# Kernel tuning notes

Hardware: AMD Instinct MI355X
Metric: run time of the kernel (lower is better)

## Reference

```python
import jax, jax.numpy as jnp
import numpy as np

EMBED = 1024
NUM_HEADS = 16
HEAD = EMBED // NUM_HEADS  # 64


def setup_inputs() -> dict:
    key = jax.random.key(0)
    kx, kk, kq, kv = jax.random.split(key, 4)
    B, T = 4, 4096
    scale = 1.0 / np.sqrt(EMBED)
    x = jax.random.normal(kx, (B, T, EMBED), dtype=jnp.float32)
    # nn.Linear(embed, head, bias=False) stores weight [head, embed]
    Wk = jax.random.normal(kk, (HEAD, EMBED), dtype=jnp.float32) * scale
    Wq = jax.random.normal(kq, (HEAD, EMBED), dtype=jnp.float32) * scale
    Wv = jax.random.normal(kv, (HEAD, EMBED), dtype=jnp.float32) * scale
    return {"x": x, "Wk": Wk, "Wq": Wq, "Wv": Wv}


def reference(x, Wk, Wq, Wv):
    # x: [B, T, C]; W*: [H, C] (torch Linear layout, y = x @ W.T)
    k = jnp.einsum('btc,hc->bth', x, Wk)  # [B, T, H]
    q = jnp.einsum('btc,hc->bth', x, Wq)
    v = jnp.einsum('btc,hc->bth', x, Wv)
    scale = k.shape[-1] ** -0.5
    wei = jnp.einsum('bth,bsh->bts', q, k) * scale  # [B, T, T]
    wei = jax.nn.softmax(wei, axis=-1)  # no causal mask in source
    out = jnp.einsum('bts,bsh->bth', wei, v)  # [B, T, H]
    return out
```

## Files before the change

kernel.cpp:

```cpp
#include <hip/hip_runtime.h>
#include <hip/hip_bf16.h>
#include <cstdint>

#define TSEQ 4096
#define NB   4
#define HD   64
#define CEMB 1024
#define NQ   8
#define KVCH (TSEQ / NQ)
#define NTOK (NB * TSEQ)
#define SCL  0.18033688011112042f
#define FM   16.0f

typedef __attribute__((ext_vector_type(8)))  short bfrag;
typedef __attribute__((ext_vector_type(4)))  float f4;
typedef __attribute__((ext_vector_type(16))) float f16v;

#define MFMA16(a, b, c) __builtin_amdgcn_mfma_f32_16x16x32_bf16(a, b, c, 0, 0, 0)
#define MFMA32(a, b, c) __builtin_amdgcn_mfma_f32_32x32x16_bf16(a, b, c, 0, 0, 0)

static __device__ __forceinline__ unsigned short f2bf(float f) {
    __hip_bfloat16 h = __float2bfloat16(f);
    return __builtin_bit_cast(unsigned short, h);
}

static __device__ __forceinline__ float bf2f(unsigned short u) {
    const unsigned v = (unsigned)u << 16;
    return __builtin_bit_cast(float, v);
}

static __device__ __forceinline__ unsigned cvtpk(float lo, float hi) {
    unsigned r;
    asm("v_cvt_pk_bf16_f32 %0, %1, %2" : "=v"(r) : "v"(lo), "v"(hi));
    return r;
}

static __device__ __forceinline__ bfrag cvt8pk(const float4 a, const float4 b) {
    uint4 o;
    o.x = cvtpk(a.x, a.y);
    o.y = cvtpk(a.z, a.w);
    o.z = cvtpk(b.x, b.y);
    o.w = cvtpk(b.z, b.w);
    return __builtin_bit_cast(bfrag, o);
}


__global__ __launch_bounds__(256) void wcvt_kernel(
    const float* __restrict__ Wq, const float* __restrict__ Wk,
    const float* __restrict__ Wv, unsigned short* __restrict__ wb)
{
    const int row = blockIdx.x;
    const int col = threadIdx.x * 4;
    const float* W = (row < 64) ? Wq + (size_t)row * CEMB
                   : (row < 128) ? Wk + (size_t)(row - 64) * CEMB
                   : Wv + (size_t)(row - 128) * CEMB;
    const float4 v = *reinterpret_cast<const float4*>(W + col);
    ushort4 o;
    o.x = f2bf(v.x); o.y = f2bf(v.y); o.z = f2bf(v.z); o.w = f2bf(v.w);
    *reinterpret_cast<ushort4*>(wb + (size_t)row * CEMB + col) = o;
}

__global__ __launch_bounds__(256) void proj_kernel(
    const float* __restrict__ x, const unsigned short* __restrict__ wb,
    unsigned short* __restrict__ qb, unsigned short* __restrict__ kf,
    unsigned short* __restrict__ vf)
{
    __shared__ __attribute__((aligned(16))) unsigned short xs[2][32 * 64];
    __shared__ __attribute__((aligned(16))) unsigned short ws[2][192 * 64];

    const int tid  = threadIdx.x;
    const int w    = tid >> 6;
    const int lane = tid & 63;
    const int ln15 = lane & 15, lg = lane >> 4;
    const int rowg = (w >> 1) * 16;
    const int colg = (w & 1) * 96;
    const int rowbase = blockIdx.x * 32;

    f4 acc[6];
    #pragma unroll
    for (int j = 0; j < 6; ++j) acc[j] = f4{0.f, 0.f, 0.f, 0.f};

    const int xrow = tid >> 3;
    const int xs8  = tid & 7;
    const int xswz = (xrow & 7) << 4;

    float4 xf0, xf1;
    bfrag  wf[6];
    auto LOADP = [&](int k0) {
        const float* xsrc = x + (size_t)(rowbase + xrow) * CEMB + k0 + xs8 * 8;
        xf0 = reinterpret_cast<const float4*>(xsrc)[0];
        xf1 = reinterpret_cast<const float4*>(xsrc)[1];
        #pragma unroll
        for (int i = 0; i < 6; ++i) {
            const int seg = tid + i * 256;
            const int srow = seg >> 3, sc = seg & 7;
            wf[i] = *reinterpret_cast<const bfrag*>(wb + (size_t)srow * CEMB + k0 + sc * 8);
        }
    };
    auto WRITEP = [&](int c) {
        char* xd = (char*)xs[c];
        char* wd = (char*)ws[c];
        const bfrag xb = cvt8pk(xf0, xf1);
        *reinterpret_cast<bfrag*>(xd + xrow * 128 + ((xs8 * 16) ^ xswz)) = xb;
        #pragma unroll
        for (int i = 0; i < 6; ++i) {
            const int seg = tid + i * 256;
            const int srow = seg >> 3, sc = seg & 7;
            *reinterpret_cast<bfrag*>(wd + srow * 128 + ((sc * 16) ^ ((srow & 7) << 4))) = wf[i];
        }
    };

    LOADP(0);
    WRITEP(0);
    __syncthreads();

    for (int ch = 0; ch < 16; ++ch) {
        const int c = ch & 1;
        if (ch < 15) LOADP((ch + 1) * 64);

        const char* xp = (const char*)xs[c];
        const char* wp = (const char*)ws[c];
        __builtin_amdgcn_s_setprio(1);
        #pragma unroll
        for (int ks = 0; ks < 2; ++ks) {
            const int cb = ks * 64 + lg * 16;
            const int r0 = rowg + ln15;
            const bfrag a0 = *reinterpret_cast<const bfrag*>(xp + r0 * 128 + (cb ^ ((r0 & 7) << 4)));
            #pragma unroll
            for (int ct = 0; ct < 6; ++ct) {
                const int wr = colg + ct * 16 + ln15;
                const bfrag b = *reinterpret_cast<const bfrag*>(wp + wr * 128 + (cb ^ ((wr & 7) << 4)));
                acc[ct] = MFMA16(a0, b, acc[ct]);
            }
        }
        __builtin_amdgcn_s_setprio(0);

        if (ch < 15) WRITEP(c ^ 1);
        __syncthreads();
    }

    #pragma unroll
    for (int ct = 0; ct < 6; ++ct) {
        const int c = colg + ct * 16 + ln15;
        #pragma unroll
        for (int r = 0; r < 4; ++r) {
            const int grow = rowbase + rowg + 4 * lg + r;
            const int bbi = grow >> 12, t = grow & 4095;
            const int tile = t >> 6, kvr = t & 63;
            if (c < 64) {
                qb[(size_t)grow * HD + c] = f2bf(acc[ct][r] * SCL);
            } else if (c < 128) {
                const int d = c - 64;
                const unsigned short bv16 = f2bf(acc[ct][r]);
                const int lane2 = (kvr & 31) + 32 * ((d >> 3) & 1);
                const size_t idx =
                    ((((size_t)bbi * 64 + tile) * 4 + (d >> 4)) * 2 + (kvr >> 5)) * 512
                    + lane2 * 8 + (d & 7);
                kf[idx] = bv16;
            } else {
                const int d = c - 128;
                const unsigned short bv16 = f2bf(acc[ct][r]);
                const int lane2 = (d & 31) + 32 * ((kvr >> 3) & 1);
                const size_t idx =
                    ((((size_t)bbi * 64 + tile) * 4 + (kvr >> 4)) * 2 + (d >> 5)) * 512
                    + lane2 * 8 + (kvr & 7);
                vf[idx] = bv16;
            }
        }
    }
}

__global__ __launch_bounds__(256, 3) void attn_kernel(
    const unsigned short* __restrict__ qb, const unsigned short* __restrict__ kf,
    const unsigned short* __restrict__ vf, uint2* __restrict__ po2,
    float* __restrict__ pl)
{
    __shared__ __attribute__((aligned(16))) unsigned short kl[2][4096];
    __shared__ __attribute__((aligned(16))) unsigned short vl[2][4096];

    const int tid  = threadIdx.x;
    const int w    = tid >> 6;
    const int lane = tid & 63;
    const int ql   = lane & 31;
    const int hi   = lane >> 5;
    const int chunk = blockIdx.x;
    const int xg    = blockIdx.y;
    const int q0   = xg * 128 + w * 32;
    const int bb   = xg >> 5;
    const int tbase = bb * 64 + chunk * 8;

    bfrag aq[4];
    #pragma unroll
    for (int s = 0; s < 4; ++s)
        aq[s] = *reinterpret_cast<const bfrag*>(
            qb + (size_t)(q0 + ql) * HD + 16 * s + 8 * hi);

    const unsigned short* kg = kf + (size_t)tbase * 4096 + tid * 8;
    const unsigned short* vg = vf + (size_t)tbase * 4096 + tid * 8;

    bfrag sk0, sk1, sv0, sv1;
    auto LOADT = [&](int it) {
        const size_t o = (size_t)it * 4096;
        sk0 = *reinterpret_cast<const bfrag*>(kg + o);
        sk1 = *reinterpret_cast<const bfrag*>(kg + o + 2048);
        sv0 = *reinterpret_cast<const bfrag*>(vg + o);
        sv1 = *reinterpret_cast<const bfrag*>(vg + o + 2048);
    };
    auto WRITET = [&](int c) {
        *reinterpret_cast<bfrag*>(&kl[c][tid * 8]) = sk0;
        *reinterpret_cast<bfrag*>(&kl[c][2048 + tid * 8]) = sk1;
        *reinterpret_cast<bfrag*>(&vl[c][tid * 8]) = sv0;
        *reinterpret_cast<bfrag*>(&vl[c][2048 + tid * 8]) = sv1;
    };

    auto mkpa = [&](const f16v& p, const int u0) -> bfrag {
        unsigned a0 = cvtpk(p[4 * u0 + 0], p[4 * u0 + 1]);
        unsigned a1 = cvtpk(p[4 * u0 + 2], p[4 * u0 + 3]);
        unsigned b0 = cvtpk(p[4 * u0 + 4], p[4 * u0 + 5]);
        unsigned b1 = cvtpk(p[4 * u0 + 6], p[4 * u0 + 7]);
        asm("v_permlane32_swap_b32 %0, %1" : "+v"(a0), "+v"(b0));
        asm("v_permlane32_swap_b32 %0, %1" : "+v"(a1), "+v"(b1));
        const uint4 u = make_uint4(a0, a1, b0, b1);
        return __builtin_bit_cast(bfrag, u);
    };

    f16v o0, o1;
    #pragma unroll
    for (int i = 0; i < 16; ++i) { o0[i] = 0.f; o1[i] = 0.f; }
    float lsum = 0.f;

    const int NIT = KVCH / 64;
    LOADT(0);
    WRITET(0);
    __syncthreads();

    for (int it = 0; it < NIT; ++it) {
        const int c = it & 1;
        if (it < NIT - 1) LOADT(it + 1);

        const char* kbh = (const char*)&kl[c][0];
        const char* vbh = (const char*)&vl[c][0];

        f16v s0v, s1v;
        #pragma unroll
        for (int i = 0; i < 16; ++i) { s0v[i] = -FM; s1v[i] = -FM; }
        __builtin_amdgcn_s_setprio(1);
        #pragma unroll
        for (int s = 0; s < 4; ++s) {
            const bfrag ka = *reinterpret_cast<const bfrag*>(kbh + (2 * s) * 1024 + lane * 16);
            const bfrag kc = *reinterpret_cast<const bfrag*>(kbh + (2 * s + 1) * 1024 + lane * 16);
            s0v = MFMA32(ka, aq[s], s0v);
            s1v = MFMA32(kc, aq[s], s1v);
        }
        __builtin_amdgcn_s_setprio(0);

        #pragma unroll
        for (int i = 0; i < 16; ++i) {
            s0v[i] = __builtin_amdgcn_exp2f(s0v[i]);
            s1v[i] = __builtin_amdgcn_exp2f(s1v[i]);
        }

        const bfrag pa0 = mkpa(s0v, 0);
        const bfrag pa1 = mkpa(s0v, 2);
        const bfrag pa2 = mkpa(s1v, 0);
        const bfrag pa3 = mkpa(s1v, 2);

        __builtin_amdgcn_s_setprio(1);
        {
            const bfrag va0 = *reinterpret_cast<const bfrag*>(vbh + 0 * 1024 + lane * 16);
            const bfrag vc0 = *reinterpret_cast<const bfrag*>(vbh + 1 * 1024 + lane * 16);
            o0 = MFMA32(va0, pa0, o0);  o1 = MFMA32(vc0, pa0, o1);
            const bfrag va1 = *reinterpret_cast<const bfrag*>(vbh + 2 * 1024 + lane * 16);
            const bfrag vc1 = *reinterpret_cast<const bfrag*>(vbh + 3 * 1024 + lane * 16);
            o0 = MFMA32(va1, pa1, o0);  o1 = MFMA32(vc1, pa1, o1);
            const bfrag va2 = *reinterpret_cast<const bfrag*>(vbh + 4 * 1024 + lane * 16);
            const bfrag vc2 = *reinterpret_cast<const bfrag*>(vbh + 5 * 1024 + lane * 16);
            o0 = MFMA32(va2, pa2, o0);  o1 = MFMA32(vc2, pa2, o1);
            const bfrag va3 = *reinterpret_cast<const bfrag*>(vbh + 6 * 1024 + lane * 16);
            const bfrag vc3 = *reinterpret_cast<const bfrag*>(vbh + 7 * 1024 + lane * 16);
            o0 = MFMA32(va3, pa3, o0);  o1 = MFMA32(vc3, pa3, o1);
        }
        __builtin_amdgcn_s_setprio(0);

        float a[16];
        #pragma unroll
        for (int i = 0; i < 16; ++i) a[i] = s0v[i] + s1v[i];
        #pragma unroll
        for (int st = 8; st > 0; st >>= 1)
            #pragma unroll
            for (int i = 0; i < 8; ++i) if (i < st) a[i] += a[i + st];
        lsum += a[0];

        if (it < NIT - 1) {
            WRITET(c ^ 1);
            __syncthreads();
        }
    }

    lsum += __shfl_xor(lsum, 32);

    const int wid = chunk * 512 + xg * 4 + w;
    uint2* pw = po2 + ((size_t)wid * 8) * 64 + lane;
    #pragma unroll
    for (int u = 0; u < 4; ++u) {
        uint2 w0, w1;
        w0.x = cvtpk(o0[4 * u + 0], o0[4 * u + 1]);
        w0.y = cvtpk(o0[4 * u + 2], o0[4 * u + 3]);
        pw[(size_t)u * 64] = w0;
        w1.x = cvtpk(o1[4 * u + 0], o1[4 * u + 1]);
        w1.y = cvtpk(o1[4 * u + 2], o1[4 * u + 3]);
        pw[(size_t)(4 + u) * 64] = w1;
    }
    if (hi == 0) {
        pl[chunk * NTOK + q0 + ql] = lsum;
    }
}

__global__ __launch_bounds__(256) void merge_kernel(
    const uint2* __restrict__ po2, const float* __restrict__ pl,
    float* __restrict__ out)
{
    const int t    = blockIdx.x * 256 + threadIdx.x;
    const int lane = t & 63;
    const int slot = (t >> 6) & 7;
    const int xgw  = t >> 9;
    const int row  = (xgw >> 2) * 128 + (xgw & 3) * 32 + (lane & 31);
    const int d0   = (slot >> 2) * 32 + (slot & 3) * 8 + (lane >> 5) * 4;

    float lt = 0.f;
    f4 acc = {0.f, 0.f, 0.f, 0.f};
    #pragma unroll
    for (int q = 0; q < NQ; ++q) {
        lt += pl[q * NTOK + row];
        const uint2 v = po2[((size_t)(q * 512 + xgw) * 8 + slot) * 64 + lane];
        acc[0] += bf2f((unsigned short)(v.x & 0xffffu));
        acc[1] += bf2f((unsigned short)(v.x >> 16));
        acc[2] += bf2f((unsigned short)(v.y & 0xffffu));
        acc[3] += bf2f((unsigned short)(v.y >> 16));
    }
    const float inv = 1.0f / lt;
    f4 r = { acc[0] * inv, acc[1] * inv, acc[2] * inv, acc[3] * inv };
    *reinterpret_cast<f4*>(out + (size_t)row * HD + d0) = r;
}

extern "C" void kernel_launch(void* const* d_in, const int* in_sizes, int n_in,
                              void* d_out, int out_size, void* d_ws, size_t ws_size,
                              hipStream_t stream) {
    (void)in_sizes; (void)n_in; (void)out_size; (void)ws_size;
    const float* x  = (const float*)d_in[0];
    const float* Wk = (const float*)d_in[1];
    const float* Wq = (const float*)d_in[2];
    const float* Wv = (const float*)d_in[3];

    unsigned short* qb = (unsigned short*)d_ws;
    unsigned short* kf = qb + (size_t)NTOK * HD;
    unsigned short* vf = kf + (size_t)NTOK * HD;
    unsigned short* wb = vf + (size_t)NTOK * HD;
    uint2* po2 = (uint2*)(wb + (size_t)192 * CEMB);
    float* pl  = (float*)(po2 + (size_t)NQ * 512 * 8 * 64);

    wcvt_kernel<<<192, 256, 0, stream>>>(Wq, Wk, Wv, wb);
    proj_kernel<<<512, 256, 0, stream>>>(x, wb, qb, kf, vf);
    attn_kernel<<<dim3(NQ, 128), 256, 0, stream>>>(qb, kf, vf, po2, pl);
    merge_kernel<<<1024, 256, 0, stream>>>(po2, pl, (float*)d_out);
}
```

Baseline: 52.83 us.

## Process two 32-row query tiles per wave to reuse K/V LDS fragments

Each wave now handles 64 query rows, as two 32-row tiles, instead of 32, so each K and V fragment read from LDS feeds twice as many MFMAs. The grid shrinks to 64 query groups and launch bounds drop to 2 blocks per SM to make room for the extra accumulators. The merge indexing is updated to the new partial layout. This halves K/V global and LDS traffic per query, but raises register pressure and lowers occupancy and total block count (512 blocks), which may hurt latency hiding.

```diff
diff --git a/kernel.cpp b/kernel.cpp
--- a/kernel.cpp
+++ b/kernel.cpp
@@ -170,7 +170,7 @@
     }
 }
 
-__global__ __launch_bounds__(256, 3) void attn_kernel(
+__global__ __launch_bounds__(256, 2) void attn_kernel(
     const unsigned short* __restrict__ qb, const unsigned short* __restrict__ kf,
     const unsigned short* __restrict__ vf, uint2* __restrict__ po2,
     float* __restrict__ pl)
@@ -185,15 +185,19 @@
     const int hi   = lane >> 5;
     const int chunk = blockIdx.x;
     const int xg    = blockIdx.y;
-    const int q0   = xg * 128 + w * 32;
-    const int bb   = xg >> 5;
+    const int q0A  = xg * 256 + w * 64;
+    const int q0B  = q0A + 32;
+    const int bb   = xg >> 4;
     const int tbase = bb * 64 + chunk * 8;
 
-    bfrag aq[4];
-    #pragma unroll
-    for (int s = 0; s < 4; ++s)
-        aq[s] = *reinterpret_cast<const bfrag*>(
-            qb + (size_t)(q0 + ql) * HD + 16 * s + 8 * hi);
+    bfrag aqA[4], aqB[4];
+    #pragma unroll
+    for (int s = 0; s < 4; ++s) {
+        aqA[s] = *reinterpret_cast<const bfrag*>(
+            qb + (size_t)(q0A + ql) * HD + 16 * s + 8 * hi);
+        aqB[s] = *reinterpret_cast<const bfrag*>(
+            qb + (size_t)(q0B + ql) * HD + 16 * s + 8 * hi);
+    }
 
     const unsigned short* kg = kf + (size_t)tbase * 4096 + tid * 8;
     const unsigned short* vg = vf + (size_t)tbase * 4096 + tid * 8;
@@ -224,10 +228,12 @@
         return __builtin_bit_cast(bfrag, u);
     };
 
-    f16v o0, o1;
-    #pragma unroll
-    for (int i = 0; i < 16; ++i) { o0[i] = 0.f; o1[i] = 0.f; }
-    float lsum = 0.f;
+    f16v o0A, o1A, o0B, o1B;
+    #pragma unroll
+    for (int i = 0; i < 16; ++i) {
+        o0A[i] = 0.f; o1A[i] = 0.f; o0B[i] = 0.f; o1B[i] = 0.f;
+    }
+    float lsumA = 0.f, lsumB = 0.f;
 
     const int NIT = KVCH / 64;
     LOADT(0);
@@ -241,55 +247,71 @@
         const char* kbh = (const char*)&kl[c][0];
         const char* vbh = (const char*)&vl[c][0];
 
-        f16v s0v, s1v;
-        #pragma unroll
-        for (int i = 0; i < 16; ++i) { s0v[i] = -FM; s1v[i] = -FM; }
+        f16v s0A, s1A, s0B, s1B;
+        #pragma unroll
+        for (int i = 0; i < 16; ++i) {
+            s0A[i] = -FM; s1A[i] = -FM; s0B[i] = -FM; s1B[i] = -FM;
+        }
         __builtin_amdgcn_s_setprio(1);
         #pragma unroll
         for (int s = 0; s < 4; ++s) {
             const bfrag ka = *reinterpret_cast<const bfrag*>(kbh + (2 * s) * 1024 + lane * 16);
             const bfrag kc = *reinterpret_cast<const bfrag*>(kbh + (2 * s + 1) * 1024 + lane * 16);
-            s0v = MFMA32(ka, aq[s], s0v);
-            s1v = MFMA32(kc, aq[s], s1v);
+            s0A = MFMA32(ka, aqA[s], s0A);
+            s0B = MFMA32(ka, aqB[s], s0B);
+            s1A = MFMA32(kc, aqA[s], s1A);
+            s1B = MFMA32(kc, aqB[s], s1B);
         }
         __builtin_amdgcn_s_setprio(0);
 
         #pragma unroll
         for (int i = 0; i < 16; ++i) {
-            s0v[i] = __builtin_amdgcn_exp2f(s0v[i]);
-            s1v[i] = __builtin_amdgcn_exp2f(s1v[i]);
-        }
-
-        const bfrag pa0 = mkpa(s0v, 0);
-        const bfrag pa1 = mkpa(s0v, 2);
-        const bfrag pa2 = mkpa(s1v, 0);
-        const bfrag pa3 = mkpa(s1v, 2);
+            s0A[i] = __builtin_amdgcn_exp2f(s0A[i]);
+            s1A[i] = __builtin_amdgcn_exp2f(s1A[i]);
+            s0B[i] = __builtin_amdgcn_exp2f(s0B[i]);
+            s1B[i] = __builtin_amdgcn_exp2f(s1B[i]);
+        }
+
+        const bfrag paA0 = mkpa(s0A, 0);
+        const bfrag paA1 = mkpa(s0A, 2);
+        const bfrag paA2 = mkpa(s1A, 0);
+        const bfrag paA3 = mkpa(s1A, 2);
+        const bfrag paB0 = mkpa(s0B, 0);
+        const bfrag paB1 = mkpa(s0B, 2);
+        const bfrag paB2 = mkpa(s1B, 0);
+        const bfrag paB3 = mkpa(s1B, 2);
 
         __builtin_amdgcn_s_setprio(1);
         {
             const bfrag va0 = *reinterpret_cast<const bfrag*>(vbh + 0 * 1024 + lane * 16);
             const bfrag vc0 = *reinterpret_cast<const bfrag*>(vbh + 1 * 1024 + lane * 16);
-            o0 = MFMA32(va0, pa0, o0);  o1 = MFMA32(vc0, pa0, o1);
+            o0A = MFMA32(va0, paA0, o0A);  o1A = MFMA32(vc0, paA0, o1A);
+            o0B = MFMA32(va0, paB0, o0B);  o1B = MFMA32(vc0, paB0, o1B);
             const bfrag va1 = *reinterpret_cast<const bfrag*>(vbh + 2 * 1024 + lane * 16);
             const bfrag vc1 = *reinterpret_cast<const bfrag*>(vbh + 3 * 1024 + lane * 16);
-            o0 = MFMA32(va1, pa1, o0);  o1 = MFMA32(vc1, pa1, o1);
+            o0A = MFMA32(va1, paA1, o0A);  o1A = MFMA32(vc1, paA1, o1A);
+            o0B = MFMA32(va1, paB1, o0B);  o1B = MFMA32(vc1, paB1, o1B);
             const bfrag va2 = *reinterpret_cast<const bfrag*>(vbh + 4 * 1024 + lane * 16);
             const bfrag vc2 = *reinterpret_cast<const bfrag*>(vbh + 5 * 1024 + lane * 16);
-            o0 = MFMA32(va2, pa2, o0);  o1 = MFMA32(vc2, pa2, o1);
+            o0A = MFMA32(va2, paA2, o0A);  o1A = MFMA32(vc2, paA2, o1A);
+            o0B = MFMA32(va2, paB2, o0B);  o1B = MFMA32(vc2, paB2, o1B);
             const bfrag va3 = *reinterpret_cast<const bfrag*>(vbh + 6 * 1024 + lane * 16);
             const bfrag vc3 = *reinterpret_cast<const bfrag*>(vbh + 7 * 1024 + lane * 16);
-            o0 = MFMA32(va3, pa3, o0);  o1 = MFMA32(vc3, pa3, o1);
+            o0A = MFMA32(va3, paA3, o0A);  o1A = MFMA32(vc3, paA3, o1A);
+            o0B = MFMA32(va3, paB3, o0B);  o1B = MFMA32(vc3, paB3, o1B);
         }
         __builtin_amdgcn_s_setprio(0);
 
-        float a[16];
-        #pragma unroll
-        for (int i = 0; i < 16; ++i) a[i] = s0v[i] + s1v[i];
+        float a[16], b[16];
+        #pragma unroll
+        for (int i = 0; i < 16; ++i) { a[i] = s0A[i] + s1A[i]; b[i] = s0B[i] + s1B[i]; }
         #pragma unroll
         for (int st = 8; st > 0; st >>= 1)
             #pragma unroll
-            for (int i = 0; i < 8; ++i) if (i < st) a[i] += a[i + st];
-        lsum += a[0];
+            for (int i = 0; i < 8; ++i)
+                if (i < st) { a[i] += a[i + st]; b[i] += b[i + st]; }
+        lsumA += a[0];
+        lsumB += b[0];
 
         if (it < NIT - 1) {
             WRITET(c ^ 1);
@@ -297,22 +319,31 @@
         }
     }
 
-    lsum += __shfl_xor(lsum, 32);
-
-    const int wid = chunk * 512 + xg * 4 + w;
-    uint2* pw = po2 + ((size_t)wid * 8) * 64 + lane;
+    lsumA += __shfl_xor(lsumA, 32);
+    lsumB += __shfl_xor(lsumB, 32);
+
+    const int gA = xg * 8 + w * 2;
+    uint2* pwA = po2 + ((size_t)(chunk * 512 + gA) * 8) * 64 + lane;
+    uint2* pwB = po2 + ((size_t)(chunk * 512 + gA + 1) * 8) * 64 + lane;
     #pragma unroll
     for (int u = 0; u < 4; ++u) {
-        uint2 w0, w1;
-        w0.x = cvtpk(o0[4 * u + 0], o0[4 * u + 1]);
-        w0.y = cvtpk(o0[4 * u + 2], o0[4 * u + 3]);
-        pw[(size_t)u * 64] = w0;
-        w1.x = cvtpk(o1[4 * u + 0], o1[4 * u + 1]);
-        w1.y = cvtpk(o1[4 * u + 2], o1[4 * u + 3]);
-        pw[(size_t)(4 + u) * 64] = w1;
+        uint2 wv;
+        wv.x = cvtpk(o0A[4 * u + 0], o0A[4 * u + 1]);
+        wv.y = cvtpk(o0A[4 * u + 2], o0A[4 * u + 3]);
+        pwA[(size_t)u * 64] = wv;
+        wv.x = cvtpk(o1A[4 * u + 0], o1A[4 * u + 1]);
+        wv.y = cvtpk(o1A[4 * u + 2], o1A[4 * u + 3]);
+        pwA[(size_t)(4 + u) * 64] = wv;
+        wv.x = cvtpk(o0B[4 * u + 0], o0B[4 * u + 1]);
+        wv.y = cvtpk(o0B[4 * u + 2], o0B[4 * u + 3]);
+        pwB[(size_t)u * 64] = wv;
+        wv.x = cvtpk(o1B[4 * u + 0], o1B[4 * u + 1]);
+        wv.y = cvtpk(o1B[4 * u + 2], o1B[4 * u + 3]);
+        pwB[(size_t)(4 + u) * 64] = wv;
     }
     if (hi == 0) {
-        pl[chunk * NTOK + q0 + ql] = lsum;
+        pl[chunk * NTOK + q0A + ql] = lsumA;
+        pl[chunk * NTOK + q0B + ql] = lsumB;
     }
 }
 
@@ -324,7 +355,7 @@
     const int lane = t & 63;
     const int slot = (t >> 6) & 7;
     const int xgw  = t >> 9;
-    const int row  = (xgw >> 2) * 128 + (xgw & 3) * 32 + (lane & 31);
+    const int row  = xgw * 32 + (lane & 31);
     const int d0   = (slot >> 2) * 32 + (slot & 3) * 8 + (lane >> 5) * 4;
 
     float lt = 0.f;
@@ -361,6 +392,6 @@
 
     wcvt_kernel<<<192, 256, 0, stream>>>(Wq, Wk, Wv, wb);
     proj_kernel<<<512, 256, 0, stream>>>(x, wb, qb, kf, vf);
-    attn_kernel<<<dim3(NQ, 128), 256, 0, stream>>>(qb, kf, vf, po2, pl);
+    attn_kernel<<<dim3(NQ, 64), 256, 0, stream>>>(qb, kf, vf, po2, pl);
     merge_kernel<<<1024, 256, 0, stream>>>(po2, pl, (float*)d_out);
 }
```

New measurement: 55.44 us. 4.9% more time.
